# Performance work log

Hardware: AMD Instinct MI355X
Metric: run time of the kernel (lower is better)

## Reference

```python
import jax, jax.numpy as jnp
import numpy as np

DIM = 1024
N_HEAD = 16
HEAD_DIM = DIM // N_HEAD
HIDDEN = 4 * DIM
EPS = 1e-6
NEG = -1e9


def setup_inputs() -> dict:
    key = jax.random.key(0)
    ks = jax.random.split(key, 9)
    B, T = 2, 2048
    x = jax.random.normal(ks[0], (B, T, DIM), dtype=jnp.float32)
    # additive causal mask [T, T]
    mask = jnp.where(jnp.tril(jnp.ones((T, T), dtype=bool)), 0.0, NEG).astype(jnp.float32)
    s = 0.02
    wq = jax.random.normal(ks[1], (DIM, DIM), dtype=jnp.float32) * s
    wk = jax.random.normal(ks[2], (DIM, DIM), dtype=jnp.float32) * s
    wv = jax.random.normal(ks[3], (DIM, DIM), dtype=jnp.float32) * s
    wo = jax.random.normal(ks[4], (DIM, DIM), dtype=jnp.float32) * s
    w1 = jax.random.normal(ks[5], (DIM, HIDDEN), dtype=jnp.float32) * s
    w2 = jax.random.normal(ks[6], (HIDDEN, DIM), dtype=jnp.float32) * s
    g_attn = jnp.ones((DIM,), dtype=jnp.float32)
    g_ffn = jnp.ones((DIM,), dtype=jnp.float32)
    return {"x": x, "mask": mask, "wq": wq, "wk": wk, "wv": wv, "wo": wo,
            "w1": w1, "w2": w2, "g_attn": g_attn, "g_ffn": g_ffn}


def _rmsnorm(x, g):
    norm = jax.lax.rsqrt(jnp.mean(jnp.square(x), axis=-1, keepdims=True) + EPS)
    return (x * norm) * g


def _attention(x, mask, wq, wk, wv, wo):
    B, T, C = x.shape
    # project and split heads: [B, H, T, D]
    q = (x @ wq).reshape(B, T, N_HEAD, HEAD_DIM).transpose(0, 2, 1, 3)
    k = (x @ wk).reshape(B, T, N_HEAD, HEAD_DIM).transpose(0, 2, 1, 3)
    v = (x @ wv).reshape(B, T, N_HEAD, HEAD_DIM).transpose(0, 2, 1, 3)
    attn = jnp.einsum('bhtd,bhsd->bhts', q, k) / np.sqrt(HEAD_DIM).astype(np.float32)
    attn = attn + mask  # broadcast [T,T] over [B,H,T,T]
    p = jax.nn.softmax(attn, axis=-1)
    out = jnp.einsum('bhts,bhsd->bhtd', p, v)
    out = out.transpose(0, 2, 1, 3).reshape(B, T, C)
    return out @ wo


def reference(x, mask, wq, wk, wv, wo, w1, w2, g_attn, g_ffn):
    x = x + _attention(_rmsnorm(x, g_attn), mask, wq, wk, wv, wo)
    h = _rmsnorm(x, g_ffn)
    return x + (jax.nn.silu(h @ w1) @ w2)
```

## Files before the change

kernel.cpp:

```cpp
#include <hip/hip_runtime.h>
#include <hip/hip_bf16.h>
#include <cstdint>
#include <cstddef>

#define DIM    1024
#define NHEAD  16
#define HDIM   64
#define HIDDEN 4096
#define TSEQ   2048
#define TOKENS 4096

typedef __attribute__((ext_vector_type(4))) float  f32x4;
typedef __attribute__((ext_vector_type(8))) short  short8;
typedef __attribute__((ext_vector_type(8))) __bf16 bf16x8;

__device__ __forceinline__ short f2bf(float f) {
    union { float f; uint32_t u; } v; v.f = f;
    uint32_t u = v.u;
    uint32_t r = (u + 0x7fffu + ((u >> 16) & 1u)) >> 16;
    return (short)r;
}

__device__ __forceinline__ float bf2f(short s) {
    uint32_t u = ((uint32_t)(uint16_t)s) << 16;
    return __builtin_bit_cast(float, u);
}

__device__ __forceinline__ f32x4 mfma_bf16(short8 a, short8 b, f32x4 c) {
    return __builtin_amdgcn_mfma_f32_16x16x32_bf16(
        __builtin_bit_cast(bf16x8, a), __builtin_bit_cast(bf16x8, b), c, 0, 0, 0);
}

__device__ __forceinline__ void barrier_lds() {
    asm volatile("s_waitcnt lgkmcnt(0)\n\ts_barrier" ::: "memory");
}

__global__ __launch_bounds__(256) void transpose_w(
    const float* __restrict__ W, short* __restrict__ Wt, int K, int N)
{
    __shared__ float tile[64][65];
    const int tid = threadIdx.x;
    const int n0 = blockIdx.x * 64, k0 = blockIdx.y * 64;
    for (int i = tid; i < 4096; i += 256) {
        int r = i >> 6, c = i & 63;
        tile[r][c] = W[(size_t)(k0 + r) * N + n0 + c];
    }
    __syncthreads();
    for (int i = tid; i < 4096; i += 256) {
        int r = i >> 6, c = i & 63;
        Wt[(size_t)(n0 + r) * K + k0 + c] = f2bf(tile[c][r]);
    }
}

__global__ __launch_bounds__(256) void transpose_v(
    const short* __restrict__ qkv, short* __restrict__ Vt)
{
    __shared__ short tile[64][72];
    const int tid = threadIdx.x;
    const int s0 = blockIdx.x * 64, bh = blockIdx.y;
    const int b = bh >> 4, h = bh & 15;
    const short* src = qkv + ((size_t)(b * TSEQ + s0)) * 3072 + 2048 + h * 64;
    for (int i = tid; i < 512; i += 256) {
        int r = i >> 3, cg = i & 7;
        *(short8*)&tile[r][cg * 8] = *(const short8*)(src + (size_t)r * 3072 + cg * 8);
    }
    __syncthreads();
    short* dst = Vt + ((size_t)bh * 64) * TSEQ + s0;
    for (int i = tid; i < 512; i += 256) {
        int d = i >> 3, sg = i & 7;
        short8 o;
#pragma unroll
        for (int j = 0; j < 8; ++j) o[j] = tile[sg * 8 + j][d];
        *(short8*)(dst + (size_t)d * TSEQ + sg * 8) = o;
    }
}

__global__ __launch_bounds__(256) void rmsnorm_k(
    const float* __restrict__ x, const float* __restrict__ g, short* __restrict__ out)
{
    const int t = blockIdx.x, tid = threadIdx.x;
    const int wave = tid >> 6, lane = tid & 63;
    const float4 v = ((const float4*)(x + (size_t)t * DIM))[tid];
    float ss = v.x * v.x + v.y * v.y + v.z * v.z + v.w * v.w;
#pragma unroll
    for (int d = 1; d < 64; d <<= 1) ss += __shfl_xor(ss, d, 64);
    __shared__ float red[4];
    if (lane == 0) red[wave] = ss;
    __syncthreads();
    float tot = red[0] + red[1] + red[2] + red[3];
    float rn = rsqrtf(tot * (1.0f / (float)DIM) + 1e-6f);
    const float4 gv = ((const float4*)g)[tid];
    short4 ov = make_short4(f2bf(v.x * rn * gv.x), f2bf(v.y * rn * gv.y),
                            f2bf(v.z * rn * gv.z), f2bf(v.w * rn * gv.w));
    ((short4*)(out + (size_t)t * DIM))[tid] = ov;
}

template <int EPI>
__global__ __launch_bounds__(256) void gemm_bt(
    const short* __restrict__ A, const short* __restrict__ Bt,
    void* __restrict__ Cout, const float* __restrict__ res,
    int M, int N, int K)
{
    __shared__ short As[128 * 64];
    __shared__ short Bs[128 * 64];
    const int tid  = threadIdx.x;
    const int wave = tid >> 6, lane = tid & 63;
    const int lm = lane & 15, quad = lane >> 4;
    const int wm = wave & 1, wn = wave >> 1;
    const int m0 = blockIdx.x * 128, n0 = blockIdx.y * 128;
    const int Ksl = K / gridDim.z;
    const int kbeg = blockIdx.z * Ksl;
    const int nIter = Ksl >> 6;

    const f32x4 zero = {0.f, 0.f, 0.f, 0.f};
    f32x4 acc[4][4];
#pragma unroll
    for (int i = 0; i < 4; ++i)
#pragma unroll
        for (int j = 0; j < 4; ++j) acc[i][j] = zero;

    const int srow = tid >> 3;
    const int scol = (tid & 7) * 8;
    const int pcol = ((tid & 7) ^ (srow & 7)) * 8;
    const short* Ap = A + (size_t)(m0 + srow) * K + kbeg + scol;
    const short* Bp = Bt + (size_t)(n0 + srow) * K + kbeg + scol;

    short8 ar[4], br[4];

    auto loadtile = [&]() {
#pragma unroll
        for (int j = 0; j < 4; ++j) {
            ar[j] = *(const short8*)(Ap + (size_t)(j * 32) * K);
            br[j] = *(const short8*)(Bp + (size_t)(j * 32) * K);
        }
        Ap += 64; Bp += 64;
    };

    auto storetile = [&]() {
#pragma unroll
        for (int j = 0; j < 4; ++j) {
            *(short8*)&As[(srow + j * 32) * 64 + pcol] = ar[j];
            *(short8*)&Bs[(srow + j * 32) * 64 + pcol] = br[j];
        }
    };

    const int e = lm & 7;
    auto compute = [&]() {
#pragma unroll
        for (int kk = 0; kk < 2; ++kk) {
            short8 af[4], bf[4];
#pragma unroll
            for (int mt = 0; mt < 4; ++mt)
                af[mt] = *(const short8*)&As[(wm * 64 + mt * 16 + lm) * 64 +
                                             ((((kk << 2) | quad) ^ e) << 3)];
#pragma unroll
            for (int nt = 0; nt < 4; ++nt)
                bf[nt] = *(const short8*)&Bs[(wn * 64 + nt * 16 + lm) * 64 +
                                             ((((kk << 2) | quad) ^ e) << 3)];
#pragma unroll
            for (int mt = 0; mt < 4; ++mt)
#pragma unroll
                for (int nt = 0; nt < 4; ++nt)
                    acc[mt][nt] = mfma_bf16(af[mt], bf[nt], acc[mt][nt]);
        }
    };

    loadtile();

    for (int it = 0; it < nIter; ++it) {
        barrier_lds();
        storetile();
        barrier_lds();
        if (it + 1 < nIter) loadtile();
        compute();
    }

#pragma unroll
    for (int mt = 0; mt < 4; ++mt) {
#pragma unroll
        for (int r = 0; r < 4; ++r) {
            const int row = m0 + wm * 64 + mt * 16 + quad * 4 + r;
#pragma unroll
            for (int nt = 0; nt < 4; ++nt) {
                const int col = n0 + wn * 64 + nt * 16 + lm;
                const size_t idx = (size_t)row * N + col;
                const float v = acc[mt][nt][r];
                if constexpr (EPI == 0) {
                    ((short*)Cout)[idx] = f2bf(v);
                } else if constexpr (EPI == 1) {
                    ((float*)Cout)[idx] = res[idx] + v;
                } else if constexpr (EPI == 2) {
                    ((short*)Cout)[idx] = f2bf(v / (1.0f + __expf(-v)));
                } else {
                    ((short*)Cout)[(size_t)blockIdx.z * M * N + idx] = f2bf(v);
                }
            }
        }
    }
}

__global__ __launch_bounds__(256) void combine_k4(
    const short* __restrict__ p, const float* __restrict__ res,
    float* __restrict__ out, int n)
{
    const int i = blockIdx.x * 256 + threadIdx.x;
    if (i * 4 < n) {
        float4 v = ((const float4*)res)[i];
#pragma unroll
        for (int s = 0; s < 4; ++s) {
            short4 ps = ((const short4*)(p + (size_t)s * n))[i];
            v.x += bf2f(ps.x); v.y += bf2f(ps.y);
            v.z += bf2f(ps.z); v.w += bf2f(ps.w);
        }
        ((float4*)out)[i] = v;
    }
}

__global__ __launch_bounds__(256) void combine_rms4(
    const short* __restrict__ p, const float* __restrict__ res,
    const float* __restrict__ g, float* __restrict__ x2out,
    short* __restrict__ nout)
{
    const int t = blockIdx.x, tid = threadIdx.x;
    const int wave = tid >> 6, lane = tid & 63;
    const size_t i4 = (size_t)t * 256 + tid;
    float4 v = ((const float4*)res)[i4];
#pragma unroll
    for (int s = 0; s < 4; ++s) {
        short4 ps = ((const short4*)(p + (size_t)s * TOKENS * DIM))[i4];
        v.x += bf2f(ps.x); v.y += bf2f(ps.y);
        v.z += bf2f(ps.z); v.w += bf2f(ps.w);
    }
    ((float4*)x2out)[i4] = v;
    float ss = v.x * v.x + v.y * v.y + v.z * v.z + v.w * v.w;
#pragma unroll
    for (int d = 1; d < 64; d <<= 1) ss += __shfl_xor(ss, d, 64);
    __shared__ float red[4];
    if (lane == 0) red[wave] = ss;
    __syncthreads();
    float tot = red[0] + red[1] + red[2] + red[3];
    float rn = rsqrtf(tot * (1.0f / (float)DIM) + 1e-6f);
    const float4 gv = ((const float4*)g)[tid];
    short4 ov = make_short4(f2bf(v.x * rn * gv.x), f2bf(v.y * rn * gv.y),
                            f2bf(v.z * rn * gv.z), f2bf(v.w * rn * gv.w));
    ((short4*)nout)[i4] = ov;
}

#define LP 72
__global__ __launch_bounds__(256, 2) void attn_k(
    const short* __restrict__ qkv, const short* __restrict__ Vt,
    short* __restrict__ out)
{
    __shared__ short Ks[2][64 * LP];
    __shared__ short Vts[2][64 * LP];
    __shared__ short Ps[4][32 * LP];

    const int tid = threadIdx.x, wave = tid >> 6, lane = tid & 63;
    const int pair = wave >> 1, wv = wave & 1;
    const int lm = lane & 15, quad = lane >> 4;
    const int bh = blockIdx.x;
    const int qt = (gridDim.y - 1) - blockIdx.y;
    const int b = bh >> 4, h = bh & 15;
    const int q0 = qt * 64;

    const int n  = qt + 1;
    const int nA = (n + 1) >> 1;
    const int nP = pair ? (n >> 1) : nA;
    const int sbase = pair ? nA : 0;

    const int tp = tid & 127;
    const int rr = tp >> 3, cg = tp & 7;

    const short* qb = qkv + ((size_t)(b * TSEQ + q0)) * 3072 + h * 64;
    short8 aq[2][2];
#pragma unroll
    for (int mt = 0; mt < 2; ++mt)
#pragma unroll
        for (int kk = 0; kk < 2; ++kk)
            aq[mt][kk] = *(const short8*)(qb + (size_t)(wv * 32 + mt * 16 + lm) * 3072 + kk * 32 + quad * 8);

    const short* kb  = qkv + (size_t)b * TSEQ * 3072 + 1024 + h * 64;
    const short* vtb = Vt + (size_t)bh * 64 * TSEQ;

    const f32x4 zero = {0.f, 0.f, 0.f, 0.f};
    f32x4 o_acc[2][4];
#pragma unroll
    for (int mt = 0; mt < 2; ++mt)
#pragma unroll
        for (int t = 0; t < 4; ++t) o_acc[mt][t] = zero;
    float lsum[2][4] = {{0.f, 0.f, 0.f, 0.f}, {0.f, 0.f, 0.f, 0.f}};

    short8 kr[4], vr[4];
    if (nP > 0) {
        const size_t s0 = (size_t)sbase * 64;
#pragma unroll
        for (int j = 0; j < 4; ++j) {
            kr[j] = *(const short8*)(kb + (s0 + rr + j * 16) * 3072 + cg * 8);
            vr[j] = *(const short8*)(vtb + (size_t)(rr + j * 16) * TSEQ + s0 + cg * 8);
        }
    }

    for (int it = 0; it < nA; ++it) {
        const int st = sbase + it;
        const bool act = it < nP;
        __syncthreads();
        if (act) {
#pragma unroll
            for (int j = 0; j < 4; ++j) {
                *(short8*)&Ks[pair][(rr + j * 16) * LP + cg * 8] = kr[j];
                *(short8*)&Vts[pair][(rr + j * 16) * LP + cg * 8] = vr[j];
            }
        }
        __syncthreads();
        if (act && it + 1 < nP) {
            const size_t sn = (size_t)(st + 1) * 64;
#pragma unroll
            for (int j = 0; j < 4; ++j) {
                kr[j] = *(const short8*)(kb + (sn + rr + j * 16) * 3072 + cg * 8);
                vr[j] = *(const short8*)(vtb + (size_t)(rr + j * 16) * TSEQ + sn + cg * 8);
            }
        }
        if (!act) continue;

        f32x4 sa[2][4];
#pragma unroll
        for (int mt = 0; mt < 2; ++mt)
#pragma unroll
            for (int nt = 0; nt < 4; ++nt) sa[mt][nt] = zero;
#pragma unroll
        for (int kk = 0; kk < 2; ++kk) {
#pragma unroll
            for (int nt = 0; nt < 4; ++nt) {
                short8 bk = *(const short8*)&Ks[pair][(nt * 16 + lm) * LP + kk * 32 + quad * 8];
                sa[0][nt] = mfma_bf16(aq[0][kk], bk, sa[0][nt]);
                sa[1][nt] = mfma_bf16(aq[1][kk], bk, sa[1][nt]);
            }
        }

        const int s0 = st * 64;
        const bool band = (st == qt);
#pragma unroll
        for (int mt = 0; mt < 2; ++mt) {
            const int qrow = q0 + wv * 32 + mt * 16 + quad * 4;
#pragma unroll
            for (int nt = 0; nt < 4; ++nt) {
                const int col = s0 + nt * 16 + lm;
#pragma unroll
                for (int r = 0; r < 4; ++r) {
                    float p = __expf(0.125f * sa[mt][nt][r]);
                    if (band && col > qrow + r) p = 0.f;
                    lsum[mt][r] += p;
                    Ps[wave][(mt * 16 + quad * 4 + r) * LP + nt * 16 + lm] =
                        (short)(__builtin_bit_cast(uint32_t, p) >> 16);
                }
            }
        }

#pragma unroll
        for (int kk = 0; kk < 2; ++kk) {
            short8 ap0 = *(const short8*)&Ps[wave][lm * LP + kk * 32 + quad * 8];
            short8 ap1 = *(const short8*)&Ps[wave][(16 + lm) * LP + kk * 32 + quad * 8];
#pragma unroll
            for (int t = 0; t < 4; ++t) {
                short8 bv = *(const short8*)&Vts[pair][(t * 16 + lm) * LP + kk * 32 + quad * 8];
                o_acc[0][t] = mfma_bf16(ap0, bv, o_acc[0][t]);
                o_acc[1][t] = mfma_bf16(ap1, bv, o_acc[1][t]);
            }
        }
    }

#pragma unroll
    for (int mt = 0; mt < 2; ++mt)
#pragma unroll
        for (int r = 0; r < 4; ++r) {
            float s = lsum[mt][r];
#pragma unroll
            for (int d = 1; d < 16; d <<= 1) s += __shfl_xor(s, d, 16);
            lsum[mt][r] = s;
        }

    __syncthreads();
    float* Ob = (float*)&Ks[0][0];
    float* Lb = (float*)&Vts[0][0];
    if (pair == 1) {
#pragma unroll
        for (int mt = 0; mt < 2; ++mt)
#pragma unroll
            for (int t = 0; t < 4; ++t)
#pragma unroll
                for (int r = 0; r < 4; ++r)
                    Ob[(wv * 32 + mt * 16 + quad * 4 + r) * 68 + t * 16 + lm] = o_acc[mt][t][r];
        if (lm == 0) {
#pragma unroll
            for (int mt = 0; mt < 2; ++mt)
#pragma unroll
                for (int r = 0; r < 4; ++r)
                    Lb[wv * 32 + mt * 16 + quad * 4 + r] = lsum[mt][r];
        }
    }
    __syncthreads();
    if (pair == 0) {
#pragma unroll
        for (int mt = 0; mt < 2; ++mt) {
#pragma unroll
            for (int r = 0; r < 4; ++r) {
                const int lrow = wv * 32 + mt * 16 + quad * 4 + r;
                float ltot = lsum[mt][r] + Lb[lrow];
                const float inv = 1.0f / ltot;
                const int token = b * TSEQ + q0 + lrow;
#pragma unroll
                for (int t = 0; t < 4; ++t) {
                    float o = o_acc[mt][t][r] + Ob[lrow * 68 + t * 16 + lm];
                    out[(size_t)token * 1024 + h * 64 + t * 16 + lm] = f2bf(o * inv);
                }
            }
        }
    }
}

extern "C" void kernel_launch(void* const* d_in, const int* in_sizes, int n_in,
                              void* d_out, int out_size, void* d_ws, size_t ws_size,
                              hipStream_t stream)
{
    const float* x      = (const float*)d_in[0];
    const float* wq     = (const float*)d_in[2];
    const float* wk     = (const float*)d_in[3];
    const float* wv     = (const float*)d_in[4];
    const float* wo     = (const float*)d_in[5];
    const float* w1     = (const float*)d_in[6];
    const float* w2     = (const float*)d_in[7];
    const float* g_attn = (const float*)d_in[8];
    const float* g_ffn  = (const float*)d_in[9];
    float* out = (float*)d_out;

    char* ws = (char*)d_ws;
    const size_t MB = 1024 * 1024;
    short* Wqkv_t = (short*)(ws + 0);
    short* Wo_t   = (short*)(ws + 6 * MB);
    short* W1_t   = (short*)(ws + 8 * MB);
    short* xn     = (short*)(ws + 16 * MB);
    short* hbuf   = (short*)(ws + 24 * MB);
    short* qkv    = (short*)(ws + 32 * MB);
    short* pbufO  = (short*)(ws + 32 * MB);
    short* Vt     = (short*)(ws + 64 * MB);
    float* x2     = (float*)(ws + 64 * MB);
    short* W2_t   = (short*)(ws + 80 * MB);
    short* pbuf2  = (short*)(ws + 0);

    dim3 blk(256);

    transpose_w<<<dim3(16, 16), blk, 0, stream>>>(wq, Wqkv_t, 1024, 1024);
    transpose_w<<<dim3(16, 16), blk, 0, stream>>>(wk, Wqkv_t + (size_t)1024 * 1024, 1024, 1024);
    transpose_w<<<dim3(16, 16), blk, 0, stream>>>(wv, Wqkv_t + (size_t)2048 * 1024, 1024, 1024);
    transpose_w<<<dim3(16, 16), blk, 0, stream>>>(wo, Wo_t, 1024, 1024);
    transpose_w<<<dim3(64, 16), blk, 0, stream>>>(w1, W1_t, 1024, 4096);
    transpose_w<<<dim3(16, 64), blk, 0, stream>>>(w2, W2_t, 4096, 1024);

    rmsnorm_k<<<TOKENS, blk, 0, stream>>>(x, g_attn, xn);

    gemm_bt<0><<<dim3(TOKENS / 128, 3072 / 128), blk, 0, stream>>>(
        xn, Wqkv_t, qkv, nullptr, TOKENS, 3072, 1024);

    transpose_v<<<dim3(TSEQ / 64, 32), blk, 0, stream>>>(qkv, Vt);

    attn_k<<<dim3(32, TSEQ / 64), dim3(256), 0, stream>>>(qkv, Vt, xn);

    gemm_bt<3><<<dim3(TOKENS / 128, 1024 / 128, 4), blk, 0, stream>>>(
        xn, Wo_t, pbufO, nullptr, TOKENS, 1024, 1024);

    combine_rms4<<<TOKENS, blk, 0, stream>>>(pbufO, x, g_ffn, x2, hbuf);

    gemm_bt<2><<<dim3(TOKENS / 128, HIDDEN / 128), blk, 0, stream>>>(
        hbuf, W1_t, qkv, nullptr, TOKENS, HIDDEN, 1024);

    gemm_bt<3><<<dim3(TOKENS / 128, 1024 / 128, 4), blk, 0, stream>>>(
        qkv, W2_t, pbuf2, nullptr, TOKENS, 1024, HIDDEN);

    combine_k4<<<dim3(TOKENS * DIM / 4 / 256), blk, 0, stream>>>(
        pbuf2, x2, out, TOKENS * DIM);
}
```

Baseline: 355.7 us.

## Load V fragments directly from global into registers, drop V LDS staging

The attention kernel stops staging the transposed V tile through shared memory. Each wave now loads its MFMA B-operand fragments for V straight from global memory at the start of each iteration, which frees LDS so the launch bound can ask for three blocks per SM. The exponential is rewritten as exp2f with a prescaled constant. In exchange, V loads are no longer prefetched one iteration ahead and are duplicated across the two waves of each pair, so global-load latency may be exposed right before the PV MFMAs.

```diff
diff --git a/kernel.cpp b/kernel.cpp
--- a/kernel.cpp
+++ b/kernel.cpp
@@ -247,12 +247,11 @@
 }
 
 #define LP 72
-__global__ __launch_bounds__(256, 2) void attn_k(
+__global__ __launch_bounds__(256, 3) void attn_k(
     const short* __restrict__ qkv, const short* __restrict__ Vt,
     short* __restrict__ out)
 {
     __shared__ short Ks[2][64 * LP];
-    __shared__ short Vts[2][64 * LP];
     __shared__ short Ps[4][32 * LP];
 
     const int tid = threadIdx.x, wave = tid >> 6, lane = tid & 63;
@@ -290,35 +289,41 @@
         for (int t = 0; t < 4; ++t) o_acc[mt][t] = zero;
     float lsum[2][4] = {{0.f, 0.f, 0.f, 0.f}, {0.f, 0.f, 0.f, 0.f}};
 
-    short8 kr[4], vr[4];
+    short8 kr[4];
     if (nP > 0) {
-        const size_t s0 = (size_t)sbase * 64;
-#pragma unroll
-        for (int j = 0; j < 4; ++j) {
-            kr[j] = *(const short8*)(kb + (s0 + rr + j * 16) * 3072 + cg * 8);
-            vr[j] = *(const short8*)(vtb + (size_t)(rr + j * 16) * TSEQ + s0 + cg * 8);
-        }
+        const size_t s0i = (size_t)sbase * 64;
+#pragma unroll
+        for (int j = 0; j < 4; ++j)
+            kr[j] = *(const short8*)(kb + (s0i + rr + j * 16) * 3072 + cg * 8);
     }
 
     for (int it = 0; it < nA; ++it) {
         const int st = sbase + it;
         const bool act = it < nP;
+        const int s0 = st * 64;
         __syncthreads();
         if (act) {
 #pragma unroll
-            for (int j = 0; j < 4; ++j) {
+            for (int j = 0; j < 4; ++j)
                 *(short8*)&Ks[pair][(rr + j * 16) * LP + cg * 8] = kr[j];
-                *(short8*)&Vts[pair][(rr + j * 16) * LP + cg * 8] = vr[j];
-            }
         }
         __syncthreads();
+
+        short8 vf[8];
+        if (act) {
+#pragma unroll
+            for (int t = 0; t < 4; ++t)
+#pragma unroll
+                for (int kk = 0; kk < 2; ++kk)
+                    vf[t * 2 + kk] = *(const short8*)(vtb + (size_t)(t * 16 + lm) * TSEQ + s0 + kk * 32 + quad * 8);
+        }
+        __builtin_amdgcn_sched_barrier(0);
+
         if (act && it + 1 < nP) {
             const size_t sn = (size_t)(st + 1) * 64;
 #pragma unroll
-            for (int j = 0; j < 4; ++j) {
+            for (int j = 0; j < 4; ++j)
                 kr[j] = *(const short8*)(kb + (sn + rr + j * 16) * 3072 + cg * 8);
-                vr[j] = *(const short8*)(vtb + (size_t)(rr + j * 16) * TSEQ + sn + cg * 8);
-            }
         }
         if (!act) continue;
 
@@ -337,7 +342,6 @@
             }
         }
 
-        const int s0 = st * 64;
         const bool band = (st == qt);
 #pragma unroll
         for (int mt = 0; mt < 2; ++mt) {
@@ -347,7 +351,7 @@
                 const int col = s0 + nt * 16 + lm;
 #pragma unroll
                 for (int r = 0; r < 4; ++r) {
-                    float p = __expf(0.125f * sa[mt][nt][r]);
+                    float p = exp2f(0.18033688011112042f * sa[mt][nt][r]);
                     if (band && col > qrow + r) p = 0.f;
                     lsum[mt][r] += p;
                     Ps[wave][(mt * 16 + quad * 4 + r) * LP + nt * 16 + lm] =
@@ -362,9 +366,8 @@
             short8 ap1 = *(const short8*)&Ps[wave][(16 + lm) * LP + kk * 32 + quad * 8];
 #pragma unroll
             for (int t = 0; t < 4; ++t) {
-                short8 bv = *(const short8*)&Vts[pair][(t * 16 + lm) * LP + kk * 32 + quad * 8];
-                o_acc[0][t] = mfma_bf16(ap0, bv, o_acc[0][t]);
-                o_acc[1][t] = mfma_bf16(ap1, bv, o_acc[1][t]);
+                o_acc[0][t] = mfma_bf16(ap0, vf[t * 2 + kk], o_acc[0][t]);
+                o_acc[1][t] = mfma_bf16(ap1, vf[t * 2 + kk], o_acc[1][t]);
             }
         }
     }
@@ -381,7 +384,7 @@
 
     __syncthreads();
     float* Ob = (float*)&Ks[0][0];
-    float* Lb = (float*)&Vts[0][0];
+    float* Lb = (float*)&Ps[0][0];
     if (pair == 1) {
 #pragma unroll
         for (int mt = 0; mt < 2; ++mt)
```

After: 377.3 us. +6.1%, slower.
